# Performance work log

Measured on AMD Instinct MI355X. Metric: run time of the kernel, lower is better.

## Reference

```python
import jax, jax.numpy as jnp
import numpy as np

B, C, H, W = 4, 192, 56, 56


def setup_inputs() -> dict:
    key = jax.random.key(0)
    k1, k2, k3 = jax.random.split(key, 3)
    x = jax.random.normal(k1, (B, C, H, W), dtype=jnp.float32)
    conv_w = jax.random.normal(k2, (C, 2 * C), dtype=jnp.float32) * (1.0 / np.sqrt(2 * C))
    conv_b = jax.random.normal(k3, (C,), dtype=jnp.float32) * 0.01
    bn_gamma = jnp.ones((C,), dtype=jnp.float32)
    bn_beta = jnp.zeros((C,), dtype=jnp.float32)
    bn_mean = jnp.zeros((C,), dtype=jnp.float32)
    bn_var = jnp.ones((C,), dtype=jnp.float32)
    return {"x": x, "conv_w": conv_w, "conv_b": conv_b, "bn_gamma": bn_gamma,
            "bn_beta": bn_beta, "bn_mean": bn_mean, "bn_var": bn_var, "K": 4}


def reference(x, conv_w, conv_b, bn_gamma, bn_beta, bn_mean, bn_var, K):
    b, c, h, w = x.shape
    shifts_h = list(range(0, h, K))          # rolls along H
    shifts_w = list(range(K, w, K))          # rolls along W
    n = len(shifts_h) + len(shifts_w)
    scale = n ** (-0.5)
    # (B, n, C, H, W): all circularly shifted copies (static shift set)
    rolled = jnp.stack([jnp.roll(x, i, axis=2) for i in shifts_h] +
                       [jnp.roll(x, j, axis=3) for j in shifts_w], axis=1)
    # scores: tanh(scale * x * x_rolled), summed over channels -> (B, n, 1, H, W)
    scores = jnp.tanh(rolled * x[:, None] * scale).sum(axis=2, keepdims=True)
    weights = jax.nn.softmax(scores, axis=1)
    out = (rolled * weights).sum(axis=1)     # (B, C, H, W)
    cat = jnp.concatenate([x, out], axis=1)  # (B, 2C, H, W)
    # 1x1 conv as GEMM over channels
    y = jnp.einsum('bchw,oc->bohw', cat, conv_w) + conv_b[None, :, None, None]
    # BatchNorm2d in eval mode (running stats)
    eps = 1e-5
    inv = bn_gamma / jnp.sqrt(bn_var + eps)
    y = (y - bn_mean[None, :, None, None]) * inv[None, :, None, None] + bn_beta[None, :, None, None]
    return jax.nn.gelu(y, approximate=False)
```

## Files before the change

kernel.cpp:

```cpp
#include <hip/hip_runtime.h>
#include <hip/hip_bf16.h>
#include <hip/hip_fp16.h>
#include <math.h>

#define BB 4
#define CC 192
#define HH 56
#define WW 56
#define HWW 3136

typedef __attribute__((ext_vector_type(8))) short short8;
typedef __attribute__((ext_vector_type(4))) short short4v;
typedef __attribute__((ext_vector_type(8))) _Float16 half8;
typedef __attribute__((ext_vector_type(4))) float f32x4;

__device__ __forceinline__ unsigned short f2h(float f) {
    __half h = __float2half_rn(f);
    return __builtin_bit_cast(unsigned short, h);
}
__device__ __forceinline__ float2 h2f2(unsigned int u) {
    return __half22float2(__builtin_bit_cast(__half2, u));
}

__global__ __launch_bounds__(256) void k_pre(const float* __restrict__ x,
                                             const float* __restrict__ cw,
                                             unsigned short* __restrict__ xh16,
                                             unsigned short* __restrict__ wh16) {
    int tid = threadIdx.x, bid = blockIdx.x;
    if (bid < 2352) {
        __shared__ float tile[32][33];
        int b = bid / 588, rem = bid % 588;
        int by = rem / 98, bx = rem % 98;
        int tx = tid & 31, ty = tid >> 5;
        int p0 = bx * 32, c0 = by * 32;
#pragma unroll
        for (int i = 0; i < 4; i++) {
            int c = c0 + ty + 8 * i;
            tile[ty + 8 * i][tx] = x[(b * CC + c) * HWW + p0 + tx];
        }
        __syncthreads();
#pragma unroll
        for (int i = 0; i < 4; i++) {
            int p = p0 + ty + 8 * i;
            float v = tile[tx][ty + 8 * i];
            size_t o = (size_t)(b * HWW + p) * CC + c0 + tx;
            xh16[o] = f2h(v);
        }
    } else {
        int i = (bid - 2352) * 256 + tid;
        if (i < 384 * 192) {
            int n = i / 192, k = i % 192;
            float v = (n < 192) ? cw[n * 384 + k] : cw[(n - 192) * 384 + 192 + k];
            wh16[i] = f2h(v);
        }
    }
}

__global__ __launch_bounds__(256) void k_mid(const unsigned short* __restrict__ xh16,
                                             const unsigned short* __restrict__ wh16,
                                             float* __restrict__ sp,
                                             float* __restrict__ u,
                                             float* __restrict__ z) {
    __shared__ __align__(16) char smem[18432];
    int tid = threadIdx.x, bid = blockIdx.x;

    if (bid < 1792) {
        float* Xs = (float*)smem;
        const float K2 = 0.38490017945975050f;
        bool isH = bid < 896;
        int lid = isH ? bid : bid - 896;
        int half = lid & 1;
        int rp = (lid >> 1) & 1;
        int cb2 = lid >> 2;
        int b = cb2 / 56, l0 = cb2 % 56;
        int r0 = rp * 2;

        const unsigned short* srcq = xh16 + (size_t)(b * HWW) * CC + half * 96;
        for (int idx = tid; idx < 28 * 12; idx += 256) {
            int t2 = idx / 12, cq = idx % 12;
            int pi = (r0 + t2 / 14) + 4 * (t2 % 14);
            int pix = isH ? (pi * WW + l0) : (l0 * WW + pi);
            uint4 hv = *(const uint4*)(srcq + (size_t)pix * CC + cq * 8);
            float2 f0 = h2f2(hv.x), f1 = h2f2(hv.y);
            float2 f2v = h2f2(hv.z), f3 = h2f2(hv.w);
            *(float4*)&Xs[t2 * 100 + cq * 8]     = make_float4(f0.x, f0.y, f1.x, f1.y);
            *(float4*)&Xs[t2 * 100 + cq * 8 + 4] = make_float4(f2v.x, f2v.y, f3.x, f3.y);
        }
        __syncthreads();

        int perCls = isH ? 105 : 91;
        if (tid < 2 * perCls) {
            int cls = tid / perCls, p = tid % perCls;
            int a, bb;
            if (isH) {
                a = (int)((sqrtf((float)(8 * p + 1)) - 1.0f) * 0.5f);
                bb = p - (a * (a + 1)) / 2;
            } else {
                int ap = (int)((sqrtf((float)(8 * p + 1)) - 1.0f) * 0.5f);
                bb = p - (ap * (ap + 1)) / 2;
                a = ap + 1;
            }
            const float* pA = &Xs[(cls * 14 + a) * 100];
            const float* pB = &Xs[(cls * 14 + bb) * 100];
            float s0 = 0.f, s1 = 0.f, s2 = 0.f, s3 = 0.f;
#pragma unroll
            for (int q = 0; q < 24; q++) {
                float4 av = *(const float4*)(pA + q * 4);
                float4 bv = *(const float4*)(pB + q * 4);
                s0 += __builtin_amdgcn_rcpf(__expf(av.x * bv.x * K2) + 1.0f);
                s1 += __builtin_amdgcn_rcpf(__expf(av.y * bv.y * K2) + 1.0f);
                s2 += __builtin_amdgcn_rcpf(__expf(av.z * bv.z * K2) + 1.0f);
                s3 += __builtin_amdgcn_rcpf(__expf(av.w * bv.w * K2) + 1.0f);
            }
            float s = 96.0f - 2.0f * (s0 + s1 + s2 + s3);
            int r = r0 + cls;
            size_t base = (size_t)(half * BB + b) * HWW;
            if (isH) {
                int i1 = a - bb;
                int h1 = r + 4 * a, h2 = r + 4 * bb;
                sp[(base + h1 * WW + l0) * 32 + i1] = s;
                if (a != bb) sp[(base + h2 * WW + l0) * 32 + (14 - i1)] = s;
            } else {
                int d = a - bb;
                int w1 = r + 4 * a, w2 = r + 4 * bb;
                sp[(base + l0 * WW + w1) * 32 + 14 + (d - 1)] = s;
                sp[(base + l0 * WW + w2) * 32 + 14 + (13 - d)] = s;
            }
        }
        return;
    }

    {
        unsigned short* Ah = (unsigned short*)smem;
        unsigned short* Bh = Ah + 64 * 72;
        float* Ds = (float*)smem;
        int vb = bid - 1792;
        int bm = (vb % 196) * 64, bn = (vb / 196) * 64;
        int lane = tid & 63, wv = tid >> 6;

        f32x4 acc[4] = {{0,0,0,0},{0,0,0,0},{0,0,0,0},{0,0,0,0}};

        for (int kc = 0; kc < 3; kc++) {
#pragma unroll
            for (int r2 = 0; r2 < 2; r2++) {
                int idx = tid + r2 * 256;
                int m = idx >> 3, kq = idx & 7;
                size_t ao = (size_t)(bm + m) * CC + kc * 64 + kq * 8;
                *(short8*)&Ah[m * 72 + kq * 8] = *(const short8*)(xh16 + ao);
                size_t bo = (size_t)(bn + m) * 192 + kc * 64 + kq * 8;
                *(short8*)&Bh[m * 72 + kq * 8] = *(const short8*)(wh16 + bo);
            }
            __syncthreads();
            int n0 = wv * 16;
            int k8 = lane >> 4;
            int col = lane & 15;
#pragma unroll
            for (int ks = 0; ks < 64; ks += 32) {
                int koff = ks + k8 * 8;
                half8 bf = *(const half8*)&Bh[(n0 + col) * 72 + koff];
#pragma unroll
                for (int fm = 0; fm < 4; fm++) {
                    half8 af = *(const half8*)&Ah[(fm * 16 + col) * 72 + koff];
                    acc[fm] = __builtin_amdgcn_mfma_f32_16x16x32_f16(af, bf, acc[fm], 0, 0, 0);
                }
            }
            __syncthreads();
        }
        {
            int col = lane & 15, rowq = lane >> 4;
#pragma unroll
            for (int fm = 0; fm < 4; fm++)
#pragma unroll
                for (int rg = 0; rg < 4; rg++)
                    Ds[(fm * 16 + rowq * 4 + rg) * 68 + wv * 16 + col] = acc[fm][rg];
        }
        __syncthreads();
        {
            int c4 = tid & 15, m0 = tid >> 4;
            int cg = bn + c4 * 4;
            float* dst = (cg < 192) ? u : z;
            int cc = (cg < 192) ? cg : cg - 192;
            int cc8 = cc >> 3, ci = cc & 7;
            size_t cbase = (size_t)cc8 * 100352;
#pragma unroll
            for (int p = 0; p < 4; p++) {
                int m = m0 + p * 16;
                int gp = bm + m;
                int b = gp / HWW, pp = gp - b * HWW;
                int hh = pp / 56, ww2 = pp - hh * 56;
                int rr = hh & 3, tt2 = hh >> 2;
                size_t off = cbase + ((size_t)((b * 4 + rr) * 14 + tt2)) * 448 + ww2 * 8 + ci;
                float4 v = *(float4*)&Ds[m * 68 + c4 * 4];
                *(float4*)&dst[off] = v;
            }
        }
    }
}

__global__ __launch_bounds__(448, 1) void k_tail(const float* __restrict__ u,
                                                 const float* __restrict__ z,
                                                 const float* __restrict__ sp,
                                                 const float* __restrict__ cb,
                                                 const float* __restrict__ gma,
                                                 const float* __restrict__ bta,
                                                 const float* __restrict__ mea,
                                                 const float* __restrict__ var,
                                                 float* __restrict__ y) {
    __shared__ __align__(16) char arena[25088 + 28224];
    float* Zs = (float*)arena;
    unsigned short* W16 = (unsigned short*)(arena + 25088);
    float* Ys = (float*)(arena + 25088);

    int tid = threadIdx.x, bid = blockIdx.x;
    int th = bid & 1;
    int t1 = bid >> 1;
    int cc = t1 % 24;
    int t2 = t1 / 24;
    int r = t2 & 3;
    int b = t2 >> 2;
    int w = tid >> 3, c = tid & 7;
    int cg = cc * 8 + c;
    int hbase = r + 4 * (th * 7);

    size_t slab = ((size_t)cc * BB + b) * 4 + r;
    const float* zg = z + slab * 6272;
    const float* ug = u + slab * 6272;

    float4 zva0 = *(const float4*)(zg + tid * 8);
    float4 zva1 = *(const float4*)(zg + tid * 8 + 4);
    float4 zvb0, zvb1;
    if (tid < 336) {
        zvb0 = *(const float4*)(zg + (tid + 448) * 8);
        zvb1 = *(const float4*)(zg + (tid + 448) * 8 + 4);
    }
    float acc0[7];
#pragma unroll
    for (int tt = 0; tt < 7; tt++)
        acc0[tt] = ug[(th * 7 + tt) * 448 + tid];

    if (tid < 392) {
        int tq = tid / 56, ww = tid - tq * 56;
        int row = hbase + 4 * tq;
        size_t gp = (size_t)b * HWW + row * WW + ww;
        const float4* p0 = (const float4*)&sp[gp * 32];
        const float4* p1 = (const float4*)&sp[((size_t)(4 * HWW) + gp) * 32];
        float sc[28];
#pragma unroll
        for (int j = 0; j < 7; j++) {
            float4 a4 = p0[j], v4 = p1[j];
            sc[4 * j + 0] = a4.x + v4.x; sc[4 * j + 1] = a4.y + v4.y;
            sc[4 * j + 2] = a4.z + v4.z; sc[4 * j + 3] = a4.w + v4.w;
        }
        float mx = -1e30f;
#pragma unroll
        for (int s = 0; s < 27; s++) mx = fmaxf(mx, sc[s]);
        float sum = 0.f;
#pragma unroll
        for (int s = 0; s < 27; s++) { sc[s] = __expf(sc[s] - mx); sum += sc[s]; }
        float inv = __builtin_amdgcn_rcpf(sum);
        unsigned short hw[28];
#pragma unroll
        for (int s = 0; s < 27; s++) hw[s] = f2h(sc[s] * inv);
        hw[27] = 0;
        unsigned short* d = &W16[tid * 36];
        *(short8*)(d)      = *(short8*)&hw[0];
        *(short8*)(d + 8)  = *(short8*)&hw[8];
        *(short8*)(d + 16) = *(short8*)&hw[16];
        *(short4v*)(d + 24) = *(short4v*)&hw[24];
    }

    {
        float* dst = &Zs[tid * 8];
        *(float4*)dst = zva0;
        *(float4*)(dst + 4) = zva1;
    }
    if (tid < 336) {
        float* dst = &Zs[(tid + 448) * 8];
        *(float4*)dst = zvb0;
        *(float4*)(dst + 4) = zvb1;
    }
    __syncthreads();

    float zc[14];
#pragma unroll
    for (int m = 0; m < 14; m++) {
        int t0 = m + th * 7;
        if (t0 >= 14) t0 -= 14;
        zc[m] = Zs[(t0 * 56 + w) * 8 + c];
    }

    float bias = cb[cg];
    float ginv = gma[cg] * rsqrtf(var[cg] + 1e-5f);
    float bt = bta[cg];
    float me = mea[cg];

    float vout[7];
#pragma unroll
    for (int tt = 0; tt < 7; tt++) {
        int t = th * 7 + tt;
        int pb = (tt * 56 + w) * 36;
        const uint2* wp = (const uint2*)&W16[pb];
        float wt[28];
#pragma unroll
        for (int j = 0; j < 7; j++) {
            uint2 rr2 = wp[j];
            float2 fa = h2f2(rr2.x), fb = h2f2(rr2.y);
            wt[4 * j + 0] = fa.x; wt[4 * j + 1] = fa.y;
            wt[4 * j + 2] = fb.x; wt[4 * j + 3] = fb.y;
        }
        float a = acc0[tt];
#pragma unroll
        for (int i = 0; i < 14; i++)
            a += wt[i] * zc[(tt - i + 28) % 14];
#pragma unroll
        for (int j = 1; j <= 13; j++) {
            int wj = w - 4 * j; if (wj < 0) wj += 56;
            a += wt[13 + j] * Zs[(t * 56 + wj) * 8 + c];
        }
        float v = (a + bias - me) * ginv + bt;
        vout[tt] = 0.5f * v * (1.0f + erff(v * 0.70710678118654752f));
    }

    __syncthreads();
#pragma unroll
    for (int tt = 0; tt < 7; tt++)
        Ys[tt * 448 + c * 56 + w] = vout[tt];
    __syncthreads();
    {
        int c_out = tid / 56, w_out = tid - c_out * 56;
        size_t ybase = ((size_t)(b * CC + cc * 8 + c_out)) * HWW + w_out;
#pragma unroll
        for (int tt = 0; tt < 7; tt++)
            y[ybase + (size_t)(hbase + 4 * tt) * 56] = Ys[tt * 448 + c_out * 56 + w_out];
    }
}

extern "C" void kernel_launch(void* const* d_in, const int* in_sizes, int n_in,
                              void* d_out, int out_size, void* d_ws, size_t ws_size,
                              hipStream_t stream) {
    const float* x   = (const float*)d_in[0];
    const float* cw  = (const float*)d_in[1];
    const float* cb  = (const float*)d_in[2];
    const float* gma = (const float*)d_in[3];
    const float* bta = (const float*)d_in[4];
    const float* mea = (const float*)d_in[5];
    const float* var = (const float*)d_in[6];
    float* out = (float*)d_out;

    float* ws = (float*)d_ws;
    float*          sp   = ws;
    float*          u    = ws + 802816;
    float*          z    = ws + 3211264;
    unsigned short* xh16 = (unsigned short*)(ws + 5619712);
    unsigned short* wh16 = (unsigned short*)(ws + 6823936);

    k_pre<<<2640, 256, 0, stream>>>(x, cw, xh16, wh16);
    k_mid<<<2968, 256, 0, stream>>>(xh16, wh16, sp, u, z);
    k_tail<<<768, 448, 0, stream>>>(u, z, sp, cb, gma, bta, mea, var, out);
}
```

Baseline: 118.7 us.

## Store z intermediate in fp16 and defer softmax normalization in tail kernel

The second half of the GEMM output (z) is now written as fp16 instead of fp32, halving its global traffic and the tail kernel's shared-memory tile. The softmax in the tail writes unnormalized exponentials and applies the reciprocal sum once after accumulation, which removes the temporary score array and one multiply per weight. The smaller LDS footprint and a raised launch-bounds occupancy hint allow more blocks per CU. Storing z in fp16 adds rounding error to the mixing step, and unnormalized exponentials stored in fp16 could lose precision.

```diff
diff --git a/kernel.cpp b/kernel.cpp
--- a/kernel.cpp
+++ b/kernel.cpp
@@ -18,8 +18,14 @@
     __half h = __float2half_rn(f);
     return __builtin_bit_cast(unsigned short, h);
 }
+__device__ __forceinline__ float h2f1(unsigned short u) {
+    return __half2float(__builtin_bit_cast(__half, u));
+}
 __device__ __forceinline__ float2 h2f2(unsigned int u) {
     return __half22float2(__builtin_bit_cast(__half2, u));
+}
+__device__ __forceinline__ unsigned int packh2(float a, float b) {
+    return (unsigned int)f2h(a) | ((unsigned int)f2h(b) << 16);
 }
 
 __global__ __launch_bounds__(256) void k_pre(const float* __restrict__ x,
@@ -60,7 +66,7 @@
                                              const unsigned short* __restrict__ wh16,
                                              float* __restrict__ sp,
                                              float* __restrict__ u,
-                                             float* __restrict__ z) {
+                                             unsigned short* __restrict__ zh16) {
     __shared__ __align__(16) char smem[18432];
     int tid = threadIdx.x, bid = blockIdx.x;
 
@@ -178,8 +184,8 @@
         {
             int c4 = tid & 15, m0 = tid >> 4;
             int cg = bn + c4 * 4;
-            float* dst = (cg < 192) ? u : z;
-            int cc = (cg < 192) ? cg : cg - 192;
+            bool isU = (bn < 192);
+            int cc = isU ? cg : cg - 192;
             int cc8 = cc >> 3, ci = cc & 7;
             size_t cbase = (size_t)cc8 * 100352;
 #pragma unroll
@@ -191,14 +197,19 @@
                 int rr = hh & 3, tt2 = hh >> 2;
                 size_t off = cbase + ((size_t)((b * 4 + rr) * 14 + tt2)) * 448 + ww2 * 8 + ci;
                 float4 v = *(float4*)&Ds[m * 68 + c4 * 4];
-                *(float4*)&dst[off] = v;
-            }
-        }
-    }
-}
-
-__global__ __launch_bounds__(448, 1) void k_tail(const float* __restrict__ u,
-                                                 const float* __restrict__ z,
+                if (isU) {
+                    *(float4*)&u[off] = v;
+                } else {
+                    unsigned short hv[4] = {f2h(v.x), f2h(v.y), f2h(v.z), f2h(v.w)};
+                    *(short4v*)&zh16[off] = *(short4v*)hv;
+                }
+            }
+        }
+    }
+}
+
+__global__ __launch_bounds__(448, 7) void k_tail(const float* __restrict__ u,
+                                                 const unsigned short* __restrict__ zh16,
                                                  const float* __restrict__ sp,
                                                  const float* __restrict__ cb,
                                                  const float* __restrict__ gma,
@@ -206,10 +217,10 @@
                                                  const float* __restrict__ mea,
                                                  const float* __restrict__ var,
                                                  float* __restrict__ y) {
-    __shared__ __align__(16) char arena[25088 + 28224];
-    float* Zs = (float*)arena;
-    unsigned short* W16 = (unsigned short*)(arena + 25088);
-    float* Ys = (float*)(arena + 25088);
+    __shared__ __align__(16) char arena[40768];
+    unsigned short* Zs = (unsigned short*)arena;
+    unsigned short* W16 = (unsigned short*)(arena + 12544);
+    float* Ys = (float*)(arena + 12544);
 
     int tid = threadIdx.x, bid = blockIdx.x;
     int th = bid & 1;
@@ -223,16 +234,12 @@
     int hbase = r + 4 * (th * 7);
 
     size_t slab = ((size_t)cc * BB + b) * 4 + r;
-    const float* zg = z + slab * 6272;
+    const unsigned short* zg = zh16 + slab * 6272;
     const float* ug = u + slab * 6272;
 
-    float4 zva0 = *(const float4*)(zg + tid * 8);
-    float4 zva1 = *(const float4*)(zg + tid * 8 + 4);
-    float4 zvb0, zvb1;
-    if (tid < 336) {
-        zvb0 = *(const float4*)(zg + (tid + 448) * 8);
-        zvb1 = *(const float4*)(zg + (tid + 448) * 8 + 4);
-    }
+    uint4 zva = *(const uint4*)(zg + tid * 8);
+    uint4 zvb;
+    if (tid < 336) zvb = *(const uint4*)(zg + (tid + 448) * 8);
     float acc0[7];
 #pragma unroll
     for (int tt = 0; tt < 7; tt++)
@@ -244,41 +251,41 @@
         size_t gp = (size_t)b * HWW + row * WW + ww;
         const float4* p0 = (const float4*)&sp[gp * 32];
         const float4* p1 = (const float4*)&sp[((size_t)(4 * HWW) + gp) * 32];
-        float sc[28];
+        float mx = -1e30f;
 #pragma unroll
         for (int j = 0; j < 7; j++) {
             float4 a4 = p0[j], v4 = p1[j];
-            sc[4 * j + 0] = a4.x + v4.x; sc[4 * j + 1] = a4.y + v4.y;
-            sc[4 * j + 2] = a4.z + v4.z; sc[4 * j + 3] = a4.w + v4.w;
-        }
-        float mx = -1e30f;
-#pragma unroll
-        for (int s = 0; s < 27; s++) mx = fmaxf(mx, sc[s]);
+            mx = fmaxf(mx, a4.x + v4.x);
+            mx = fmaxf(mx, a4.y + v4.y);
+            mx = fmaxf(mx, a4.z + v4.z);
+            if (j < 6) mx = fmaxf(mx, a4.w + v4.w);
+        }
+        unsigned short* d = &W16[tid * 36];
         float sum = 0.f;
-#pragma unroll
-        for (int s = 0; s < 27; s++) { sc[s] = __expf(sc[s] - mx); sum += sc[s]; }
+        float e26 = 0.f;
+#pragma unroll
+        for (int j = 0; j < 7; j++) {
+            float4 a4 = p0[j], v4 = p1[j];
+            float e0 = __expf(a4.x + v4.x - mx);
+            float e1 = __expf(a4.y + v4.y - mx);
+            float e2 = __expf(a4.z + v4.z - mx);
+            if (j < 6) {
+                float e3 = __expf(a4.w + v4.w - mx);
+                sum += (e0 + e1) + (e2 + e3);
+                *(unsigned int*)&d[4 * j]     = packh2(e0, e1);
+                *(unsigned int*)&d[4 * j + 2] = packh2(e2, e3);
+            } else {
+                sum += (e0 + e1) + e2;
+                *(unsigned int*)&d[24] = packh2(e0, e1);
+                e26 = e2;
+            }
+        }
         float inv = __builtin_amdgcn_rcpf(sum);
-        unsigned short hw[28];
-#pragma unroll
-        for (int s = 0; s < 27; s++) hw[s] = f2h(sc[s] * inv);
-        hw[27] = 0;
-        unsigned short* d = &W16[tid * 36];
-        *(short8*)(d)      = *(short8*)&hw[0];
-        *(short8*)(d + 8)  = *(short8*)&hw[8];
-        *(short8*)(d + 16) = *(short8*)&hw[16];
-        *(short4v*)(d + 24) = *(short4v*)&hw[24];
-    }
-
-    {
-        float* dst = &Zs[tid * 8];
-        *(float4*)dst = zva0;
-        *(float4*)(dst + 4) = zva1;
-    }
-    if (tid < 336) {
-        float* dst = &Zs[(tid + 448) * 8];
-        *(float4*)dst = zvb0;
-        *(float4*)(dst + 4) = zvb1;
-    }
+        *(unsigned int*)&d[26] = packh2(e26, inv);
+    }
+
+    *(uint4*)&Zs[tid * 8] = zva;
+    if (tid < 336) *(uint4*)&Zs[(tid + 448) * 8] = zvb;
     __syncthreads();
 
     float zc[14];
@@ -286,7 +293,7 @@
     for (int m = 0; m < 14; m++) {
         int t0 = m + th * 7;
         if (t0 >= 14) t0 -= 14;
-        zc[m] = Zs[(t0 * 56 + w) * 8 + c];
+        zc[m] = h2f1(Zs[(t0 * 56 + w) * 8 + c]);
     }
 
     float bias = cb[cg];
@@ -308,15 +315,16 @@
             wt[4 * j + 0] = fa.x; wt[4 * j + 1] = fa.y;
             wt[4 * j + 2] = fb.x; wt[4 * j + 3] = fb.y;
         }
-        float a = acc0[tt];
+        float s = 0.f;
 #pragma unroll
         for (int i = 0; i < 14; i++)
-            a += wt[i] * zc[(tt - i + 28) % 14];
+            s += wt[i] * zc[(tt - i + 28) % 14];
 #pragma unroll
         for (int j = 1; j <= 13; j++) {
             int wj = w - 4 * j; if (wj < 0) wj += 56;
-            a += wt[13 + j] * Zs[(t * 56 + wj) * 8 + c];
-        }
+            s += wt[13 + j] * h2f1(Zs[(t * 56 + wj) * 8 + c]);
+        }
+        float a = acc0[tt] + s * wt[27];
         float v = (a + bias - me) * ginv + bt;
         vout[tt] = 0.5f * v * (1.0f + erff(v * 0.70710678118654752f));
     }
@@ -350,11 +358,11 @@
     float* ws = (float*)d_ws;
     float*          sp   = ws;
     float*          u    = ws + 802816;
-    float*          z    = ws + 3211264;
-    unsigned short* xh16 = (unsigned short*)(ws + 5619712);
-    unsigned short* wh16 = (unsigned short*)(ws + 6823936);
+    unsigned short* zh16 = (unsigned short*)(ws + 3211264);
+    unsigned short* xh16 = (unsigned short*)(ws + 4415488);
+    unsigned short* wh16 = (unsigned short*)(ws + 5619712);
 
     k_pre<<<2640, 256, 0, stream>>>(x, cw, xh16, wh16);
-    k_mid<<<2968, 256, 0, stream>>>(xh16, wh16, sp, u, z);
-    k_tail<<<768, 448, 0, stream>>>(u, z, sp, cb, gma, bta, mea, var, out);
-}
+    k_mid<<<2968, 256, 0, stream>>>(xh16, wh16, sp, u, zh16);
+    k_tail<<<768, 448, 0, stream>>>(u, zh16, sp, cb, gma, bta, mea, var, out);
+}
```

Measured after the change: 129.9 us. 1.09x slower.
